# Kernel tuning notes

Measured on AMD Instinct MI355X. Metric: run time of the kernel, lower is better.

Reference implementation:

```python
import jax, jax.numpy as jnp
import numpy as np

N = 100000   # nodes
E = 1600000  # edges (avg degree 16)
D = 128      # input_dim = embedding_dim = output_dim
NEG_SLOPE = 0.01  # nn.LeakyReLU default


def setup_inputs() -> dict:
    key = jax.random.key(0)
    k0, k1, k2, k3, k4, k5 = jax.random.split(key, 6)
    x = jax.random.normal(k0, (N, D), jnp.float32)
    edge_index = jax.random.randint(k1, (2, E), 0, N, dtype=jnp.int32)
    batch = jnp.zeros((N,), jnp.int32)
    # GCNConv params (glorot-ish scale)
    W1 = jax.random.normal(k2, (D, D), jnp.float32) * 0.05
    b1 = jax.random.normal(k3, (D,), jnp.float32) * 0.05
    W2 = jax.random.normal(k4, (D, D), jnp.float32) * 0.05
    b2 = jax.random.normal(k5, (D,), jnp.float32) * 0.05
    return {"x": x, "W1": W1, "b1": b1, "W2": W2, "b2": b2,
            "edge_index": edge_index, "batch": batch}


def _gcn_conv(x, W, b, src, dst, deg_isqrt):
    # x' = D^{-1/2} (A + I) D^{-1/2} (x W) + b   (PyG GCNConv defaults)
    h = x @ W                                   # [N, D]
    coef = deg_isqrt[src] * deg_isqrt[dst]      # [E]
    msg = h[src] * coef[:, None]                # [E, D] gather + scale
    out = jax.ops.segment_sum(msg, dst, num_segments=N)  # scatter-add
    out = out + h * (deg_isqrt * deg_isqrt)[:, None]      # self-loop term
    return out + b


def reference(x, W1, b1, W2, b2, edge_index, batch):
    src, dst = edge_index[0], edge_index[1]
    # degree on A + I (self loops), same for both layers
    deg = jax.ops.segment_sum(jnp.ones((E,), x.dtype), dst, num_segments=N) + 1.0
    deg_isqrt = jax.lax.rsqrt(deg)
    h = _gcn_conv(x, W1, b1, src, dst, deg_isqrt)
    h = jax.nn.leaky_relu(h, NEG_SLOPE)
    h = _gcn_conv(h, W2, b2, src, dst, deg_isqrt)
    return jax.nn.leaky_relu(h, NEG_SLOPE)
```

## Files before the change

kernel.cpp:

```cpp
#include <hip/hip_runtime.h>
#include <hip/hip_bf16.h>
#include <stdint.h>

#define NN 100000
#define NE 1600000
#define NR (NE + NN)
#define DD 128
#define NEG 0.01f
#define NB 196
#define EPB 4096
#define NBLK1 391

typedef __attribute__((ext_vector_type(8))) short short8;
typedef __attribute__((ext_vector_type(4))) float floatx4;
typedef __attribute__((ext_vector_type(4))) uint32_t uint32x4;

__device__ __forceinline__ uint16_t f2bf(float f){
  uint32_t i = __float_as_uint(f);
  return (uint16_t)((i + 0x7FFFu + ((i >> 16) & 1u)) >> 16);
}
__device__ __forceinline__ float lrelu(float x){ return fmaxf(x, NEG * x); }

__global__ void k_detect(const uint32_t* __restrict__ xw, int* __restrict__ flag){
  int lane = threadIdx.x;
  uint32_t w = xw[lane];
  uint32_t e = (w >> 7) & 0xFFu;
  int plaus = (e >= 100u && e <= 134u) ? 1 : 0;
  unsigned long long b = __ballot(plaus);
  if (lane == 0) flag[0] = (__popcll(b) >= 48) ? 0 : 1;
}

__global__ __launch_bounds__(256) void k_hist(const int* __restrict__ dst,
                                              int* __restrict__ ghist){
  __shared__ int lh[NB];
  int t = threadIdx.x, b = blockIdx.x;
  if (t < NB) lh[t] = 0;
  __syncthreads();
  #pragma unroll
  for (int i = 0; i < 16; i++){
    int e = b * EPB + i * 256 + t;
    if (e < NE) atomicAdd(&lh[dst[e] >> 9], 1);
  }
  __syncthreads();
  if (t < NB) ghist[t * NBLK1 + b] = lh[t];
}

__global__ __launch_bounds__(512) void k_bscan(int* __restrict__ ghist,
                                               int* __restrict__ btotal){
  __shared__ int sm[512];
  int t = threadIdx.x, bkt = blockIdx.x;
  int v = (t < NBLK1) ? ghist[bkt * NBLK1 + t] : 0;
  sm[t] = v;
  __syncthreads();
  for (int s = 1; s < 512; s <<= 1){
    int add = (t >= s) ? sm[t - s] : 0;
    __syncthreads();
    sm[t] += add;
    __syncthreads();
  }
  if (t < NBLK1) ghist[bkt * NBLK1 + t] = sm[t] - v;
  if (t == 0) btotal[bkt] = sm[511];
}

__global__ __launch_bounds__(256) void k_bscan2(const int* __restrict__ btotal,
                                                int* __restrict__ bucketbase){
  __shared__ int sm[256];
  int t = threadIdx.x;
  int v = (t < NB) ? btotal[t] : 0;
  sm[t] = v;
  __syncthreads();
  for (int s = 1; s < 256; s <<= 1){
    int add = (t >= s) ? sm[t - s] : 0;
    __syncthreads();
    sm[t] += add;
    __syncthreads();
  }
  if (t < NB) bucketbase[t] = sm[t] - v;
  if (t == 0) bucketbase[NB] = sm[255];
}

__global__ __launch_bounds__(256) void k_scatter(const int* __restrict__ src,
                                                 const int* __restrict__ dst,
                                                 const int* __restrict__ ghist,
                                                 const int* __restrict__ bucketbase,
                                                 uint64_t* __restrict__ pairs){
  __shared__ int lcur[NB];
  int t = threadIdx.x, b = blockIdx.x;
  if (t < NB) lcur[t] = bucketbase[t] + ghist[t * NBLK1 + b];
  __syncthreads();
  #pragma unroll
  for (int i = 0; i < 16; i++){
    int e = b * EPB + i * 256 + t;
    if (e < NE){
      int s = src[e], d = dst[e];
      int pos = atomicAdd(&lcur[d >> 9], 1);
      pairs[pos] = ((uint64_t)(uint32_t)d << 32) | (uint32_t)s;
    }
  }
}

__global__ __launch_bounds__(512) void k_bsort(const uint64_t* __restrict__ pairs,
                                               const int* __restrict__ bucketbase,
                                               int2* __restrict__ pairs2,
                                               int* __restrict__ prowstart,
                                               float* __restrict__ dis){
  __shared__ int lcnt[512], lofs[512], sm[512];
  __shared__ float sdn[512];
  int t = threadIdx.x, bkt = blockIdx.x;
  int n0 = bkt << 9;
  int beg = bucketbase[bkt], end = bucketbase[bkt + 1];
  int begS = beg + n0;
  lcnt[t] = 0;
  __syncthreads();
  for (int i = beg + t; i < end; i += 512){
    int d = (int)(pairs[i] >> 32);
    atomicAdd(&lcnt[d - n0], 1);
  }
  __syncthreads();
  int n = n0 + t;
  int inb = (n < NN) ? 1 : 0;
  int v = lcnt[t] + inb;
  sm[t] = v;
  __syncthreads();
  for (int s = 1; s < 512; s <<= 1){
    int add = (t >= s) ? sm[t - s] : 0;
    __syncthreads();
    sm[t] += add;
    __syncthreads();
  }
  int excl = sm[t] - v;
  float dn = rsqrtf((float)(lcnt[t] + 1));
  lofs[t] = excl + 1;
  sdn[t] = dn;
  if (inb){
    prowstart[n] = begS + excl;
    dis[n] = dn;
    pairs2[begS + excl] = make_int2(n, __float_as_int(dn));
  }
  if (bkt == 0 && t == 0) prowstart[NN] = NR;
  __syncthreads();
  for (int i = beg + t; i < end; i += 512){
    uint64_t u = pairs[i];
    int d = (int)(u >> 32);
    int p = atomicAdd(&lofs[d - n0], 1);
    pairs2[begS + p] = make_int2((int)(uint32_t)u, __float_as_int(sdn[d - n0]));
  }
}

__global__ void k_prep2(int2* __restrict__ pairs2, const float* __restrict__ dis){
  int i = blockIdx.x * 256 + threadIdx.x;
  if (i < NR){
    int2 r = pairs2[i];
    r.y = __float_as_int(__int_as_float(r.y) * dis[r.x]);
    pairs2[i] = r;
  }
}

__global__ void k_wb(const void* __restrict__ W1, const void* __restrict__ W2,
                     const void* __restrict__ b1, const void* __restrict__ b2,
                     uint16_t* __restrict__ WT1, uint16_t* __restrict__ WT2,
                     uint16_t* __restrict__ bb, const int* __restrict__ flag){
  int idx = blockIdx.x * 256 + threadIdx.x;
  int f = flag[0];
  if (idx < 16384){
    int c = idx >> 7, k = idx & 127;
    WT1[idx] = f ? f2bf(((const float*)W1)[k * DD + c])
                 : ((const uint16_t*)W1)[k * DD + c];
  } else if (idx < 32768){
    int j = idx - 16384;
    int c = j >> 7, k = j & 127;
    WT2[j] = f ? f2bf(((const float*)W2)[k * DD + c])
               : ((const uint16_t*)W2)[k * DD + c];
  } else if (idx < 33024){
    int j = idx - 32768;
    const void* s = (j < 128) ? b1 : b2;
    int i2 = j & 127;
    bb[j] = f ? f2bf(((const float*)s)[i2]) : ((const uint16_t*)s)[i2];
  }
}

__device__ __forceinline__ short8 ldcvt(const float* __restrict__ p){
  floatx4 u = ((const floatx4*)p)[0], v = ((const floatx4*)p)[1];
  short8 r;
  r[0] = (short)f2bf(u.x); r[1] = (short)f2bf(u.y);
  r[2] = (short)f2bf(u.z); r[3] = (short)f2bf(u.w);
  r[4] = (short)f2bf(v.x); r[5] = (short)f2bf(v.y);
  r[6] = (short)f2bf(v.z); r[7] = (short)f2bf(v.w);
  return r;
}

__global__ __launch_bounds__(256) void k_gemm(const void* __restrict__ X,
                                              const uint16_t* __restrict__ WT,
                                              uint16_t* __restrict__ H,
                                              const int* __restrict__ flag,
                                              int xf32){
  __shared__ uint16_t lwt[128 * 136];
  int t = threadIdx.x;
  const uint32_t* wt32 = (const uint32_t*)WT;
  #pragma unroll
  for (int i = 0; i < 32; i++){
    int uidx = t + 256 * i;
    uint32_t w2 = wt32[uidx];
    int el = uidx * 2;
    int c = el >> 7, k = el & 127;
    *(uint32_t*)&lwt[c * 136 + k] = w2;
  }
  __syncthreads();

  int wave = t >> 6, lane = t & 63;
  int m = lane & 15, q = lane >> 4;
  int rowbase = blockIdx.x * 64 + wave * 16;
  int ar = rowbase + m;
  if (ar >= NN) ar = 0;
  short8 a0, a1, a2, a3;
  if (xf32 && flag[0]){
    const float* xr = (const float*)X + (size_t)ar * DD;
    a0 = ldcvt(xr + q * 8);        a1 = ldcvt(xr + (q + 4) * 8);
    a2 = ldcvt(xr + (q + 8) * 8);  a3 = ldcvt(xr + (q + 12) * 8);
  } else {
    const short8* xrow = (const short8*)((const uint16_t*)X + (size_t)ar * DD);
    a0 = xrow[q]; a1 = xrow[q + 4]; a2 = xrow[q + 8]; a3 = xrow[q + 12];
  }

  #pragma unroll
  for (int nt = 0; nt < 8; nt++){
    int c = nt * 16 + m;
    const uint16_t* bp = &lwt[c * 136 + q * 8];
    floatx4 acc = {0.f, 0.f, 0.f, 0.f};
    acc = __builtin_amdgcn_mfma_f32_16x16x32_bf16(a0, *(const short8*)(bp +  0), acc, 0, 0, 0);
    acc = __builtin_amdgcn_mfma_f32_16x16x32_bf16(a1, *(const short8*)(bp + 32), acc, 0, 0, 0);
    acc = __builtin_amdgcn_mfma_f32_16x16x32_bf16(a2, *(const short8*)(bp + 64), acc, 0, 0, 0);
    acc = __builtin_amdgcn_mfma_f32_16x16x32_bf16(a3, *(const short8*)(bp + 96), acc, 0, 0, 0);
    #pragma unroll
    for (int r = 0; r < 4; r++){
      int row = rowbase + q * 4 + r;
      if (row < NN) H[(size_t)row * DD + c] = f2bf(acc[r]);
    }
  }
}

#define FMA8(VA, CF)                                                     \
  acc[0] = fmaf(__uint_as_float(VA.x << 16),         CF, acc[0]);        \
  acc[1] = fmaf(__uint_as_float(VA.x & 0xffff0000u), CF, acc[1]);        \
  acc[2] = fmaf(__uint_as_float(VA.y << 16),         CF, acc[2]);        \
  acc[3] = fmaf(__uint_as_float(VA.y & 0xffff0000u), CF, acc[3]);        \
  acc[4] = fmaf(__uint_as_float(VA.z << 16),         CF, acc[4]);        \
  acc[5] = fmaf(__uint_as_float(VA.z & 0xffff0000u), CF, acc[5]);        \
  acc[6] = fmaf(__uint_as_float(VA.w << 16),         CF, acc[6]);        \
  acc[7] = fmaf(__uint_as_float(VA.w & 0xffff0000u), CF, acc[7]);

__global__ __launch_bounds__(256) void k_agg(const uint16_t* __restrict__ H,
                                             const int* __restrict__ prow,
                                             const int2* __restrict__ pairs2,
                                             const uint16_t* __restrict__ bias,
                                             void* __restrict__ OUT,
                                             const int* __restrict__ flag,
                                             int is_final){
  __shared__ int2 ebuf[4][96];
  int wave = threadIdx.x >> 6, lane = threadIdx.x & 63;
  int grp = lane >> 4, sl = lane & 15;
  if (lane >= 32) ebuf[wave][32 + lane] = make_int2(0, 0);
  int n = blockIdx.x * 4 + wave;
  if (n >= NN) return;
  int beg = prow[n], end = prow[n + 1];

  float acc[8] = {0.f,0.f,0.f,0.f,0.f,0.f,0.f,0.f};
  for (int j0 = beg; j0 < end; j0 += 64){
    int cnt = min(64, end - j0);
    int2 r = (lane < cnt) ? pairs2[j0 + lane] : make_int2(0, 0);
    ebuf[wave][lane] = r;
    int chunks = (cnt + 3) >> 2;
    int2 e0 = ebuf[wave][grp];
    int2 e1 = ebuf[wave][4 + grp];
    int2 e2 = ebuf[wave][8 + grp];
    uint32x4 v0 = *(const uint32x4*)(H + (size_t)e0.x * DD + sl * 8);
    uint32x4 v1 = *(const uint32x4*)(H + (size_t)e1.x * DD + sl * 8);
    uint32x4 v2 = *(const uint32x4*)(H + (size_t)e2.x * DD + sl * 8);
    for (int c = 0; c < chunks; c += 3){
      int2 n0 = ebuf[wave][(c + 3) * 4 + grp];
      int2 n1 = ebuf[wave][(c + 4) * 4 + grp];
      int2 n2 = ebuf[wave][(c + 5) * 4 + grp];
      uint32x4 w0 = *(const uint32x4*)(H + (size_t)n0.x * DD + sl * 8);
      uint32x4 w1 = *(const uint32x4*)(H + (size_t)n1.x * DD + sl * 8);
      uint32x4 w2 = *(const uint32x4*)(H + (size_t)n2.x * DD + sl * 8);
      float c0 = __int_as_float(e0.y);
      FMA8(v0, c0)
      float c1 = __int_as_float(e1.y);
      FMA8(v1, c1)
      float c2 = __int_as_float(e2.y);
      FMA8(v2, c2)
      e0 = n0; e1 = n1; e2 = n2;
      v0 = w0; v1 = w1; v2 = w2;
    }
  }
  #pragma unroll
  for (int j = 0; j < 8; j++){
    acc[j] += __shfl_xor(acc[j], 16, 64);
    acc[j] += __shfl_xor(acc[j], 32, 64);
  }
  uint32x4 bv = ((const uint32x4*)bias)[sl];
  float o0 = lrelu(acc[0] + __uint_as_float(bv.x << 16));
  float o1 = lrelu(acc[1] + __uint_as_float(bv.x & 0xffff0000u));
  float o2 = lrelu(acc[2] + __uint_as_float(bv.y << 16));
  float o3 = lrelu(acc[3] + __uint_as_float(bv.y & 0xffff0000u));
  float o4 = lrelu(acc[4] + __uint_as_float(bv.z << 16));
  float o5 = lrelu(acc[5] + __uint_as_float(bv.z & 0xffff0000u));
  float o6 = lrelu(acc[6] + __uint_as_float(bv.w << 16));
  float o7 = lrelu(acc[7] + __uint_as_float(bv.w & 0xffff0000u));
  if (is_final && flag[0]){
    float* orow = (float*)OUT + (size_t)n * DD + sl * 8;
    if (lane < 16){ floatx4 vv = {o0, o1, o2, o3}; ((floatx4*)orow)[0] = vv; }
    else if (lane < 32){ floatx4 vv = {o4, o5, o6, o7}; ((floatx4*)orow)[1] = vv; }
  } else if (lane < 16){
    uint32x4 pv;
    pv.x = (uint32_t)f2bf(o0) | ((uint32_t)f2bf(o1) << 16);
    pv.y = (uint32_t)f2bf(o2) | ((uint32_t)f2bf(o3) << 16);
    pv.z = (uint32_t)f2bf(o4) | ((uint32_t)f2bf(o5) << 16);
    pv.w = (uint32_t)f2bf(o6) | ((uint32_t)f2bf(o7) << 16);
    *(uint32x4*)((uint16_t*)OUT + (size_t)n * DD + sl * 8) = pv;
  }
}

extern "C" void kernel_launch(void* const* d_in, const int* in_sizes, int n_in,
                              void* d_out, int out_size, void* d_ws, size_t ws_size,
                              hipStream_t stream){
  const void* x  = d_in[0];
  const void* W1 = d_in[1];
  const void* b1 = d_in[2];
  const void* W2 = d_in[3];
  const void* b2 = d_in[4];
  const int* ei   = (const int*)d_in[5];
  const int* esrc = ei;
  const int* edst = ei + NE;

  char* ws = (char*)d_ws;
  float*    dis        = (float*)(ws + 0);
  int*      prow       = (int*)(ws + 512ull * 1024);
  int*      flag       = (int*)(ws + 960ull * 1024);
  uint16_t* WT1        = (uint16_t*)(ws + 964ull * 1024);
  uint16_t* WT2        = (uint16_t*)(ws + 996ull * 1024);
  uint16_t* bb         = (uint16_t*)(ws + 1028ull * 1024);
  int*      ghist      = (int*)(ws + 1032ull * 1024);
  int*      btotal     = (int*)(ws + 1344ull * 1024);
  int*      bucketbase = (int*)(ws + 1348ull * 1024);
  int2*     pairs2     = (int2*)(ws + 2048ull * 1024);
  uint64_t* pairs      = (uint64_t*)(ws + 16384ull * 1024);
  uint16_t* hA         = (uint16_t*)(ws + 16384ull * 1024);
  uint16_t* hB         = (uint16_t*)d_out;

  k_detect<<<1, 64, 0, stream>>>((const uint32_t*)x, flag);
  k_hist  <<<NBLK1, 256, 0, stream>>>(edst, ghist);
  k_bscan <<<NB, 512, 0, stream>>>(ghist, btotal);
  k_bscan2<<<1, 256, 0, stream>>>(btotal, bucketbase);
  k_scatter<<<NBLK1, 256, 0, stream>>>(esrc, edst, ghist, bucketbase, pairs);
  k_bsort <<<NB, 512, 0, stream>>>(pairs, bucketbase, pairs2, prow, dis);
  k_prep2 <<<(NR + 255) / 256, 256, 0, stream>>>(pairs2, dis);
  k_wb    <<<129, 256, 0, stream>>>(W1, W2, b1, b2, WT1, WT2, bb, flag);

  k_gemm<<<(NN + 63) / 64, 256, 0, stream>>>(x, WT1, hA, flag, 1);
  k_agg <<<NN / 4, 256, 0, stream>>>(hA, prow, pairs2, bb, hB, flag, 0);
  k_gemm<<<(NN + 63) / 64, 256, 0, stream>>>(hB, WT2, hA, flag, 0);
  k_agg <<<NN / 4, 256, 0, stream>>>(hA, prow, pairs2, bb + 128, d_out, flag, 1);
}
```

Baseline: 312.9 us.

## Replace two-pass bucket sort CSR build with global-atomic degree count and scatter

The CSR construction used to go through a bucketed two-level sort: per-block histograms, two scans, a scatter to an intermediate pair buffer, a per-bucket local sort, and a coefficient fix-up pass. It now counts in-degrees with global atomics, scans them into row starts, and scatters each edge directly into its CSR slot through per-node atomic cursors, computing the normalisation coefficient on the fly. This drops the intermediate 64-bit pair buffer and several kernel launches. In exchange it relies on heavy global atomic contention, and the order of edges within a row becomes nondeterministic, which can change floating-point summation order.

```diff
diff --git a/kernel.cpp b/kernel.cpp
--- a/kernel.cpp
+++ b/kernel.cpp
@@ -7,9 +7,9 @@
 #define NR (NE + NN)
 #define DD 128
 #define NEG 0.01f
-#define NB 196
-#define EPB 4096
-#define NBLK1 391
+#define NBS 196
+#define NBLKE 1563
+#define NBLKZ 391
 
 typedef __attribute__((ext_vector_type(8))) short short8;
 typedef __attribute__((ext_vector_type(4))) float floatx4;
@@ -21,35 +21,38 @@
 }
 __device__ __forceinline__ float lrelu(float x){ return fmaxf(x, NEG * x); }
 
-__global__ void k_detect(const uint32_t* __restrict__ xw, int* __restrict__ flag){
-  int lane = threadIdx.x;
-  uint32_t w = xw[lane];
-  uint32_t e = (w >> 7) & 0xFFu;
-  int plaus = (e >= 100u && e <= 134u) ? 1 : 0;
-  unsigned long long b = __ballot(plaus);
-  if (lane == 0) flag[0] = (__popcll(b) >= 48) ? 0 : 1;
-}
-
-__global__ __launch_bounds__(256) void k_hist(const int* __restrict__ dst,
-                                              int* __restrict__ ghist){
-  __shared__ int lh[NB];
+__global__ __launch_bounds__(256) void k_z(int* __restrict__ deg,
+                                           const uint32_t* __restrict__ xw,
+                                           int* __restrict__ flag){
+  int i = blockIdx.x * 256 + threadIdx.x;
+  if (i < NN) deg[i] = 0;
+  if (blockIdx.x == 0 && threadIdx.x < 64){
+    int lane = threadIdx.x;
+    uint32_t w = xw[lane];
+    uint32_t e = (w >> 7) & 0xFFu;
+    int plaus = (e >= 100u && e <= 134u) ? 1 : 0;
+    unsigned long long b = __ballot(plaus);
+    if (lane == 0) flag[0] = (__popcll(b) >= 48) ? 0 : 1;
+  }
+}
+
+__global__ __launch_bounds__(256) void k_deg(const int* __restrict__ dst,
+                                             int* __restrict__ deg){
   int t = threadIdx.x, b = blockIdx.x;
-  if (t < NB) lh[t] = 0;
-  __syncthreads();
-  #pragma unroll
-  for (int i = 0; i < 16; i++){
-    int e = b * EPB + i * 256 + t;
-    if (e < NE) atomicAdd(&lh[dst[e] >> 9], 1);
-  }
-  __syncthreads();
-  if (t < NB) ghist[t * NBLK1 + b] = lh[t];
-}
-
-__global__ __launch_bounds__(512) void k_bscan(int* __restrict__ ghist,
-                                               int* __restrict__ btotal){
+  #pragma unroll
+  for (int i = 0; i < 4; i++){
+    int e = b * 1024 + i * 256 + t;
+    if (e < NE) atomicAdd(&deg[dst[e]], 1);
+  }
+}
+
+__global__ __launch_bounds__(512) void k_scan1(const int* __restrict__ deg,
+                                               int* __restrict__ prow,
+                                               int* __restrict__ bsum){
   __shared__ int sm[512];
-  int t = threadIdx.x, bkt = blockIdx.x;
-  int v = (t < NBLK1) ? ghist[bkt * NBLK1 + t] : 0;
+  int t = threadIdx.x, b = blockIdx.x;
+  int i = b * 512 + t;
+  int v = (i < NN) ? deg[i] + 1 : 0;
   sm[t] = v;
   __syncthreads();
   for (int s = 1; s < 512; s <<= 1){
@@ -58,15 +61,16 @@
     sm[t] += add;
     __syncthreads();
   }
-  if (t < NBLK1) ghist[bkt * NBLK1 + t] = sm[t] - v;
-  if (t == 0) btotal[bkt] = sm[511];
-}
-
-__global__ __launch_bounds__(256) void k_bscan2(const int* __restrict__ btotal,
-                                                int* __restrict__ bucketbase){
+  if (i < NN) prow[i] = sm[t] - v;
+  if (t == 511) bsum[b] = sm[511];
+}
+
+__global__ __launch_bounds__(256) void k_scan2(const int* __restrict__ bsum,
+                                               int* __restrict__ bbase,
+                                               int* __restrict__ prow){
   __shared__ int sm[256];
   int t = threadIdx.x;
-  int v = (t < NB) ? btotal[t] : 0;
+  int v = (t < NBS) ? bsum[t] : 0;
   sm[t] = v;
   __syncthreads();
   for (int s = 1; s < 256; s <<= 1){
@@ -75,84 +79,42 @@
     sm[t] += add;
     __syncthreads();
   }
-  if (t < NB) bucketbase[t] = sm[t] - v;
-  if (t == 0) bucketbase[NB] = sm[255];
-}
-
-__global__ __launch_bounds__(256) void k_scatter(const int* __restrict__ src,
-                                                 const int* __restrict__ dst,
-                                                 const int* __restrict__ ghist,
-                                                 const int* __restrict__ bucketbase,
-                                                 uint64_t* __restrict__ pairs){
-  __shared__ int lcur[NB];
+  if (t < NBS) bbase[t] = sm[t] - v;
+  if (t == 0) prow[NN] = NR;
+}
+
+__global__ __launch_bounds__(512) void k_scan3(const int* __restrict__ deg,
+                                               const int* __restrict__ bbase,
+                                               int* __restrict__ prow,
+                                               float* __restrict__ dis,
+                                               int* __restrict__ cursor,
+                                               int2* __restrict__ pairs2){
   int t = threadIdx.x, b = blockIdx.x;
-  if (t < NB) lcur[t] = bucketbase[t] + ghist[t * NBLK1 + b];
-  __syncthreads();
-  #pragma unroll
-  for (int i = 0; i < 16; i++){
-    int e = b * EPB + i * 256 + t;
+  int i = b * 512 + t;
+  if (i >= NN) return;
+  int p = prow[i] + bbase[b];
+  prow[i] = p;
+  float dn = rsqrtf((float)(deg[i] + 1));
+  dis[i] = dn;
+  cursor[i] = p + 1;
+  pairs2[p] = make_int2(i, __float_as_int(dn * dn));
+}
+
+__global__ __launch_bounds__(256) void k_scat(const int* __restrict__ src,
+                                              const int* __restrict__ dst,
+                                              const float* __restrict__ dis,
+                                              int* __restrict__ cursor,
+                                              int2* __restrict__ pairs2){
+  int t = threadIdx.x, b = blockIdx.x;
+  #pragma unroll
+  for (int i = 0; i < 4; i++){
+    int e = b * 1024 + i * 256 + t;
     if (e < NE){
       int s = src[e], d = dst[e];
-      int pos = atomicAdd(&lcur[d >> 9], 1);
-      pairs[pos] = ((uint64_t)(uint32_t)d << 32) | (uint32_t)s;
+      float cf = dis[d] * dis[s];
+      int pos = atomicAdd(&cursor[d], 1);
+      pairs2[pos] = make_int2(s, __float_as_int(cf));
     }
-  }
-}
-
-__global__ __launch_bounds__(512) void k_bsort(const uint64_t* __restrict__ pairs,
-                                               const int* __restrict__ bucketbase,
-                                               int2* __restrict__ pairs2,
-                                               int* __restrict__ prowstart,
-                                               float* __restrict__ dis){
-  __shared__ int lcnt[512], lofs[512], sm[512];
-  __shared__ float sdn[512];
-  int t = threadIdx.x, bkt = blockIdx.x;
-  int n0 = bkt << 9;
-  int beg = bucketbase[bkt], end = bucketbase[bkt + 1];
-  int begS = beg + n0;
-  lcnt[t] = 0;
-  __syncthreads();
-  for (int i = beg + t; i < end; i += 512){
-    int d = (int)(pairs[i] >> 32);
-    atomicAdd(&lcnt[d - n0], 1);
-  }
-  __syncthreads();
-  int n = n0 + t;
-  int inb = (n < NN) ? 1 : 0;
-  int v = lcnt[t] + inb;
-  sm[t] = v;
-  __syncthreads();
-  for (int s = 1; s < 512; s <<= 1){
-    int add = (t >= s) ? sm[t - s] : 0;
-    __syncthreads();
-    sm[t] += add;
-    __syncthreads();
-  }
-  int excl = sm[t] - v;
-  float dn = rsqrtf((float)(lcnt[t] + 1));
-  lofs[t] = excl + 1;
-  sdn[t] = dn;
-  if (inb){
-    prowstart[n] = begS + excl;
-    dis[n] = dn;
-    pairs2[begS + excl] = make_int2(n, __float_as_int(dn));
-  }
-  if (bkt == 0 && t == 0) prowstart[NN] = NR;
-  __syncthreads();
-  for (int i = beg + t; i < end; i += 512){
-    uint64_t u = pairs[i];
-    int d = (int)(u >> 32);
-    int p = atomicAdd(&lofs[d - n0], 1);
-    pairs2[begS + p] = make_int2((int)(uint32_t)u, __float_as_int(sdn[d - n0]));
-  }
-}
-
-__global__ void k_prep2(int2* __restrict__ pairs2, const float* __restrict__ dis){
-  int i = blockIdx.x * 256 + threadIdx.x;
-  if (i < NR){
-    int2 r = pairs2[i];
-    r.y = __float_as_int(__int_as_float(r.y) * dis[r.x]);
-    pairs2[i] = r;
   }
 }
 
@@ -340,22 +302,21 @@
   uint16_t* WT1        = (uint16_t*)(ws + 964ull * 1024);
   uint16_t* WT2        = (uint16_t*)(ws + 996ull * 1024);
   uint16_t* bb         = (uint16_t*)(ws + 1028ull * 1024);
-  int*      ghist      = (int*)(ws + 1032ull * 1024);
-  int*      btotal     = (int*)(ws + 1344ull * 1024);
-  int*      bucketbase = (int*)(ws + 1348ull * 1024);
+  int*      deg        = (int*)(ws + 1032ull * 1024);
+  int*      cursor     = (int*)(ws + 1440ull * 1024);
+  int*      bsum       = (int*)(ws + 1848ull * 1024);
+  int*      bbase      = (int*)(ws + 1852ull * 1024);
   int2*     pairs2     = (int2*)(ws + 2048ull * 1024);
-  uint64_t* pairs      = (uint64_t*)(ws + 16384ull * 1024);
   uint16_t* hA         = (uint16_t*)(ws + 16384ull * 1024);
   uint16_t* hB         = (uint16_t*)d_out;
 
-  k_detect<<<1, 64, 0, stream>>>((const uint32_t*)x, flag);
-  k_hist  <<<NBLK1, 256, 0, stream>>>(edst, ghist);
-  k_bscan <<<NB, 512, 0, stream>>>(ghist, btotal);
-  k_bscan2<<<1, 256, 0, stream>>>(btotal, bucketbase);
-  k_scatter<<<NBLK1, 256, 0, stream>>>(esrc, edst, ghist, bucketbase, pairs);
-  k_bsort <<<NB, 512, 0, stream>>>(pairs, bucketbase, pairs2, prow, dis);
-  k_prep2 <<<(NR + 255) / 256, 256, 0, stream>>>(pairs2, dis);
-  k_wb    <<<129, 256, 0, stream>>>(W1, W2, b1, b2, WT1, WT2, bb, flag);
+  k_z    <<<NBLKZ, 256, 0, stream>>>(deg, (const uint32_t*)x, flag);
+  k_deg  <<<NBLKE, 256, 0, stream>>>(edst, deg);
+  k_scan1<<<NBS, 512, 0, stream>>>(deg, prow, bsum);
+  k_scan2<<<1, 256, 0, stream>>>(bsum, bbase, prow);
+  k_scan3<<<NBS, 512, 0, stream>>>(deg, bbase, prow, dis, cursor, pairs2);
+  k_scat <<<NBLKE, 256, 0, stream>>>(esrc, edst, dis, cursor, pairs2);
+  k_wb   <<<129, 256, 0, stream>>>(W1, W2, b1, b2, WT1, WT2, bb, flag);
 
   k_gemm<<<(NN + 63) / 64, 256, 0, stream>>>(x, WT1, hA, flag, 1);
   k_agg <<<NN / 4, 256, 0, stream>>>(hA, prow, pairs2, bb, hB, flag, 0);
```

New measurement: 420.4 us. +34.3%, slower.
